# Optimization experiments

Measured on AMD Instinct MI355X. Metric: run time of the kernel, lower is better.

## Reference

```python
import jax, jax.numpy as jnp
import numpy as np

DIM = 128
IND_DIM = 5
HEADS = 4
DIM_HEAD = 32
HIDDEN = HEADS * DIM_HEAD  # 128
SCALE = DIM_HEAD ** -0.5


def setup_inputs() -> dict:
    key = jax.random.key(0)
    ks = jax.random.split(key, 6)
    b, n = 1, 512
    x = jax.random.normal(ks[0], (b, DIM, n), dtype=jnp.float32)
    indicator = jax.random.normal(ks[1], (b, IND_DIM, n, n), dtype=jnp.float32)
    # conv1d kernels with kernel_size=1 are just (out, in) matrices
    w_qkv = jax.random.normal(ks[2], (HIDDEN * 3, DIM), dtype=jnp.float32) * (DIM ** -0.5)
    w_ind = jax.random.normal(ks[3], (HIDDEN * 2, IND_DIM), dtype=jnp.float32) * (IND_DIM ** -0.5)
    w_out = jax.random.normal(ks[4], (DIM, HIDDEN), dtype=jnp.float32) * (HIDDEN ** -0.5)
    b_out = jax.random.normal(ks[5], (DIM,), dtype=jnp.float32) * 0.01
    return {"x": x, "indicator": indicator, "w_qkv": w_qkv,
            "w_ind": w_ind, "w_out": w_out, "b_out": b_out}


def reference(x, indicator, w_qkv, w_ind, w_out, b_out):
    b, c, n = x.shape
    h, dh = HEADS, DIM_HEAD
    # pointwise conv = channel matmul
    qkv = jnp.einsum('oc,bcn->bon', w_qkv, x)  # (b, 3*hidden, n)
    q, k, v = jnp.split(qkv, 3, axis=1)
    q = q.reshape(b, h, dh, n)
    k = k.reshape(b, h, dh, n)
    v = v.reshape(b, h, dh, n)
    ind = jnp.einsum('oc,bcij->boij', w_ind, indicator)  # (b, 2*hidden, n, n)
    ind_q, ind_k = jnp.split(ind, 2, axis=1)
    ind_q = ind_q.reshape(b, h, dh, n, n)
    ind_k = ind_k.reshape(b, h, dh, n, n)
    qq = (q[..., :, None] + ind_q) * SCALE        # (b, h, dh, n, n)
    kk = k[..., None, :] + ind_k                   # (b, h, dh, n, n)
    sim = jnp.einsum('bhdij,bhdij->bhij', qq, kk)  # (b, h, n, n)
    attn = jax.nn.softmax(sim, axis=-1)
    out = jnp.einsum('bhij,bhdj->bhdi', attn, v)   # (b, h, dh, n)
    out = out.reshape(b, h * dh, n)
    return jnp.einsum('oc,bcn->bon', w_out, out) + b_out[None, :, None]
```

## Files before the change

kernel.cpp:

```cpp
#include <hip/hip_runtime.h>
#include <hip/hip_fp16.h>
#include <math.h>

#define N      512
#define DIMC   128
#define HEADS  4
#define DH     32
#define INDC   5
#define SCALE  0.1767766952966369f

#define QKV_ROWS 384
#define AQ_BASE  384
#define AK_BASE  404
#define TOT_ROWS 424
#define NROW_BLK (TOT_ROWS / 4)

#define MHS_F    (TOT_ROWS * N / 2)
#define WOUTT_F  (MHS_F + 64)

__global__ __launch_bounds__(256) void pre_kernel(const float* __restrict__ w_qkv,
                                                  const float* __restrict__ w_ind,
                                                  const float* __restrict__ x,
                                                  const float* __restrict__ w_out,
                                                  float* __restrict__ ws) {
    const int bx = blockIdx.x;
    const int t  = threadIdx.x;
    __half* rows  = (__half*)ws;
    float* MhS    = ws + MHS_F;
    float* w_outT = ws + WOUTT_F;

    if (bx == NROW_BLK) {
        if (blockIdx.y != 0) return;
        __shared__ float mraw[HEADS * INDC * INDC];
        if (t < HEADS * INDC * INDC) {
            const int h = t / 25, c = (t / 5) % 5, cc = t % 5;
            float acc = 0.f;
            for (int d = 0; d < DH; ++d)
                acc = fmaf(w_ind[(h * DH + d) * INDC + c],
                           w_ind[(DIMC + h * DH + d) * INDC + cc], acc);
            mraw[t] = acc;
        }
        __syncthreads();
        if (t < 64) {
            const int h = t >> 4, idx = t & 15;
            const int PC[10]  = {0, 0, 0, 0, 1, 1, 1, 2, 2, 3};
            const int PCC[10] = {1, 2, 3, 4, 2, 3, 4, 3, 4, 4};
            float s = 0.f;
            if (idx < 5) {
                s = mraw[h * 25 + idx * 5 + idx];
            } else if (idx < 15) {
                const int c = PC[idx - 5], cc = PCC[idx - 5];
                s = mraw[h * 25 + c * 5 + cc] + mraw[h * 25 + cc * 5 + c];
            }
            MhS[h * 16 + idx] = s;
        }
        for (int idx = t; idx < DIMC * DIMC; idx += 256) {
            const int o = idx >> 7, c = idx & 127;
            w_outT[c * DIMC + o] = w_out[idx];
        }
        return;
    }

    __shared__ float ws2[4 * DIMC];
    const int o0 = bx * 4;
    for (int idx = t; idx < 4 * DIMC; idx += 256) {
        const int r = idx & 3, m = idx >> 2;
        const int row = o0 + r;
        float val;
        if (row < QKV_ROWS) {
            val = w_qkv[row * DIMC + m];
        } else if (row < AK_BASE) {
            const int rr = row - AQ_BASE, h = rr / INDC, c = rr % INDC;
            float acc = 0.f;
            for (int d = 0; d < DH; ++d)
                acc = fmaf(w_qkv[(h * DH + d) * DIMC + m],
                           w_ind[(DIMC + h * DH + d) * INDC + c], acc);
            val = acc;
        } else {
            const int rr = row - AK_BASE, h = rr / INDC, c = rr % INDC;
            float acc = 0.f;
            for (int d = 0; d < DH; ++d)
                acc = fmaf(w_qkv[(DIMC + h * DH + d) * DIMC + m],
                           w_ind[(h * DH + d) * INDC + c], acc);
            val = acc;
        }
        ws2[m * 4 + r] = val;
    }
    __syncthreads();

    const int i = blockIdx.y * 256 + t;
    float acc[4] = {0.f, 0.f, 0.f, 0.f};
#pragma unroll 8
    for (int c = 0; c < DIMC; ++c) {
        const float xv = x[c * N + i];
        const float4 wv = *(const float4*)(ws2 + c * 4);
        acc[0] = fmaf(wv.x, xv, acc[0]);
        acc[1] = fmaf(wv.y, xv, acc[1]);
        acc[2] = fmaf(wv.z, xv, acc[2]);
        acc[3] = fmaf(wv.w, xv, acc[3]);
    }
#pragma unroll
    for (int r = 0; r < 4; ++r) rows[(o0 + r) * N + i] = __float2half(acc[r]);
}

__global__ __launch_bounds__(256) void attn_kernel(const float* __restrict__ ws,
                                                   const float* __restrict__ ind,
                                                   const float* __restrict__ b_out,
                                                   float* __restrict__ out) {
    const int i0   = blockIdx.x * 2;
    const int t    = threadIdx.x;
    const int lane = t & 63;
    const int wave = t >> 6;

    const __half* rows  = (const __half*)ws;
    const float* MhS    = ws + MHS_F;
    const float* w_outT = ws + WOUTT_F;

    const __half* q  = rows;
    const __half* Aq = rows + 3 * DIMC * N;

    __shared__ float qs[2][DIMC];
    __shared__ float aqs[2][HEADS * INDC];
    __shared__ float msS[HEADS * 16];
    __shared__ float ps[HEADS][2][N];
    __shared__ float red[HEADS][DH][64];
    __shared__ float red4[2][HEADS][2][4];
    __shared__ float attv[2][DIMC];
    __shared__ float outred[4][2][DIMC];

    if (t < DIMC) qs[0][t] = __half2float(q[t * N + i0]);
    else          qs[1][t - DIMC] = __half2float(q[(t - DIMC) * N + i0 + 1]);
    if (t < 2 * HEADS * INDC) {
        const int ii = t / (HEADS * INDC), r = t % (HEADS * INDC);
        aqs[ii][r] = __half2float(Aq[r * N + i0 + ii]);
    } else if (t < 2 * HEADS * INDC + 64) {
        msS[t - 2 * HEADS * INDC] = MhS[t - 2 * HEADS * INDC];
    }
    __syncthreads();

    float2 ic0[INDC], ic1[INDC];
#pragma unroll
    for (int c = 0; c < INDC; ++c) {
        ic0[c] = ((const float2*)(ind + (c * N + i0) * N))[t];
        ic1[c] = ((const float2*)(ind + (c * N + i0 + 1) * N))[t];
    }
    float2 prod0[15], prod1[15];
#pragma unroll
    for (int c = 0; c < INDC; ++c) {
        prod0[c] = make_float2(ic0[c].x * ic0[c].x, ic0[c].y * ic0[c].y);
        prod1[c] = make_float2(ic1[c].x * ic1[c].x, ic1[c].y * ic1[c].y);
    }
    {
        int p = 5;
#pragma unroll
        for (int c = 0; c < INDC; ++c)
#pragma unroll
            for (int cc = c + 1; cc < INDC; ++cc, ++p) {
                prod0[p] = make_float2(ic0[c].x * ic0[cc].x, ic0[c].y * ic0[cc].y);
                prod1[p] = make_float2(ic1[c].x * ic1[cc].x, ic1[c].y * ic1[cc].y);
            }
    }

    const __half2* k2  = (const __half2*)(rows + DIMC * N);
    const __half2* Ak2 = (const __half2*)(rows + (3 * DIMC + HEADS * INDC) * N);
    float2 sim0[HEADS], sim1[HEADS];
#pragma unroll
    for (int h = 0; h < HEADS; ++h) {
        float2 qk0 = {0.f, 0.f}, qk1 = {0.f, 0.f};
#pragma unroll
        for (int d = 0; d < DH; ++d) {
            const float2 kv = __half22float2(k2[(h * DH + d) * 256 + t]);
            const float q0 = qs[0][h * DH + d], q1 = qs[1][h * DH + d];
            qk0.x = fmaf(q0, kv.x, qk0.x); qk0.y = fmaf(q0, kv.y, qk0.y);
            qk1.x = fmaf(q1, kv.x, qk1.x); qk1.y = fmaf(q1, kv.y, qk1.y);
        }
        float2 lin0 = {0.f, 0.f}, lin1 = {0.f, 0.f};
#pragma unroll
        for (int c = 0; c < INDC; ++c) {
            const float2 akv = __half22float2(Ak2[(h * INDC + c) * 256 + t]);
            const float a0 = aqs[0][h * INDC + c], a1 = aqs[1][h * INDC + c];
            lin0.x = fmaf(a0 + akv.x, ic0[c].x, lin0.x);
            lin0.y = fmaf(a0 + akv.y, ic0[c].y, lin0.y);
            lin1.x = fmaf(a1 + akv.x, ic1[c].x, lin1.x);
            lin1.y = fmaf(a1 + akv.y, ic1[c].y, lin1.y);
        }
        float2 qd0 = {0.f, 0.f}, qd1 = {0.f, 0.f};
#pragma unroll
        for (int p = 0; p < 15; ++p) {
            const float sv = msS[h * 16 + p];
            qd0.x = fmaf(sv, prod0[p].x, qd0.x); qd0.y = fmaf(sv, prod0[p].y, qd0.y);
            qd1.x = fmaf(sv, prod1[p].x, qd1.x); qd1.y = fmaf(sv, prod1[p].y, qd1.y);
        }
        sim0[h].x = SCALE * (qk0.x + lin0.x + qd0.x);
        sim0[h].y = SCALE * (qk0.y + lin0.y + qd0.y);
        sim1[h].x = SCALE * (qk1.x + lin1.x + qd1.x);
        sim1[h].y = SCALE * (qk1.y + lin1.y + qd1.y);
    }

#pragma unroll
    for (int h = 0; h < HEADS; ++h) {
        float m0 = fmaxf(sim0[h].x, sim0[h].y);
        float m1 = fmaxf(sim1[h].x, sim1[h].y);
#pragma unroll
        for (int off = 32; off; off >>= 1) {
            m0 = fmaxf(m0, __shfl_down(m0, off, 64));
            m1 = fmaxf(m1, __shfl_down(m1, off, 64));
        }
        if (lane == 0) { red4[0][h][0][wave] = m0; red4[0][h][1][wave] = m1; }
    }
    __syncthreads();
    float2 e0[HEADS], e1[HEADS];
#pragma unroll
    for (int h = 0; h < HEADS; ++h) {
        const float m0 = fmaxf(fmaxf(red4[0][h][0][0], red4[0][h][0][1]),
                               fmaxf(red4[0][h][0][2], red4[0][h][0][3]));
        const float m1 = fmaxf(fmaxf(red4[0][h][1][0], red4[0][h][1][1]),
                               fmaxf(red4[0][h][1][2], red4[0][h][1][3]));
        e0[h].x = __expf(sim0[h].x - m0); e0[h].y = __expf(sim0[h].y - m0);
        e1[h].x = __expf(sim1[h].x - m1); e1[h].y = __expf(sim1[h].y - m1);
        float s0 = e0[h].x + e0[h].y, s1 = e1[h].x + e1[h].y;
#pragma unroll
        for (int off = 32; off; off >>= 1) {
            s0 += __shfl_down(s0, off, 64);
            s1 += __shfl_down(s1, off, 64);
        }
        if (lane == 0) { red4[1][h][0][wave] = s0; red4[1][h][1][wave] = s1; }
    }
    __syncthreads();
#pragma unroll
    for (int h = 0; h < HEADS; ++h) {
        const float s0 = (red4[1][h][0][0] + red4[1][h][0][1]) +
                         (red4[1][h][0][2] + red4[1][h][0][3]);
        const float s1 = (red4[1][h][1][0] + red4[1][h][1][1]) +
                         (red4[1][h][1][2] + red4[1][h][1][3]);
        const float r0 = 1.f / s0, r1 = 1.f / s1;
        ((float2*)&ps[h][0][0])[t] = make_float2(e0[h].x * r0, e0[h].y * r0);
        ((float2*)&ps[h][1][0])[t] = make_float2(e1[h].x * r1, e1[h].y * r1);
    }
    __syncthreads();

    {
        const int h = wave;
        float acc0[DH], acc1[DH];
#pragma unroll
        for (int d = 0; d < DH; ++d) { acc0[d] = 0.f; acc1[d] = 0.f; }
        const float2* ps0 = (const float2*)&ps[h][0][0];
        const float2* ps1 = (const float2*)&ps[h][1][0];
        const __half2* v2 = (const __half2*)(rows + 2 * DIMC * N);
        for (int s = 0; s < 4; ++s) {
            const float2 p0 = ps0[lane + 64 * s];
            const float2 p1 = ps1[lane + 64 * s];
#pragma unroll
            for (int d = 0; d < DH; ++d) {
                const float2 vv = __half22float2(v2[(h * DH + d) * 256 + lane + 64 * s]);
                acc0[d] = fmaf(p0.x, vv.x, fmaf(p0.y, vv.y, acc0[d]));
                acc1[d] = fmaf(p1.x, vv.x, fmaf(p1.y, vv.y, acc1[d]));
            }
        }
        const int d = lane & 31, half = lane >> 5;
#pragma unroll
        for (int dd = 0; dd < DH; ++dd) red[h][dd][lane ^ dd] = acc0[dd];
        float s = 0.f;
#pragma unroll
        for (int kk = 0; kk < 32; ++kk) s += red[h][d][(half * 32 + kk) ^ d];
        s += __shfl_down(s, 32, 64);
        if (lane < 32) attv[0][h * DH + d] = s;
#pragma unroll
        for (int dd = 0; dd < DH; ++dd) red[h][dd][lane ^ dd] = acc1[dd];
        s = 0.f;
#pragma unroll
        for (int kk = 0; kk < 32; ++kk) s += red[h][d][(half * 32 + kk) ^ d];
        s += __shfl_down(s, 32, 64);
        if (lane < 32) attv[1][h * DH + d] = s;
    }
    __syncthreads();

    {
        const int po = t & 63;
        const int quarter = t >> 6;
        const float2* wT2 = (const float2*)w_outT;
        float2 a0 = {0.f, 0.f}, a1 = {0.f, 0.f};
#pragma unroll 8
        for (int c = quarter * 32; c < quarter * 32 + 32; ++c) {
            const float2 wv = wT2[c * 64 + po];
            const float av0 = attv[0][c], av1 = attv[1][c];
            a0.x = fmaf(wv.x, av0, a0.x); a0.y = fmaf(wv.y, av0, a0.y);
            a1.x = fmaf(wv.x, av1, a1.x); a1.y = fmaf(wv.y, av1, a1.y);
        }
        ((float2*)&outred[quarter][0][0])[po] = a0;
        ((float2*)&outred[quarter][1][0])[po] = a1;
    }
    __syncthreads();
    {
        const int o = t & 127, ii = t >> 7;
        out[o * N + i0 + ii] = ((outred[0][ii][o] + outred[1][ii][o]) +
                                (outred[2][ii][o] + outred[3][ii][o])) + b_out[o];
    }
}

extern "C" void kernel_launch(void* const* d_in, const int* in_sizes, int n_in,
                              void* d_out, int out_size, void* d_ws, size_t ws_size,
                              hipStream_t stream) {
    const float* x         = (const float*)d_in[0];
    const float* indicator = (const float*)d_in[1];
    const float* w_qkv     = (const float*)d_in[2];
    const float* w_ind     = (const float*)d_in[3];
    const float* w_out     = (const float*)d_in[4];
    const float* b_out     = (const float*)d_in[5];
    float* out = (float*)d_out;
    float* ws  = (float*)d_ws;

    pre_kernel<<<dim3(NROW_BLK + 1, 2), 256, 0, stream>>>(w_qkv, w_ind, x, w_out, ws);
    attn_kernel<<<N / 2, 256, 0, stream>>>(ws, indicator, b_out, out);
}
```

Baseline: 101.2 us.

## Assign one head per wave so softmax and PV stay in registers

Each wave now owns one head over all 512 keys, with four keys per lane loaded as float4 indicator values and packed half4 k/v. It computes the scores, the softmax with wave-level shuffles, and the PV accumulation directly from registers. This removes the shared-memory probability buffer, the cross-wave max/sum reductions and three block barriers. Normalisation is deferred to the final attention vector. In exchange, each wave recomputes the indicator products per head, and the larger per-lane register state may lower occupancy.

```diff
diff --git a/kernel.cpp b/kernel.cpp
--- a/kernel.cpp
+++ b/kernel.cpp
@@ -110,24 +110,32 @@
     const int i0   = blockIdx.x * 2;
     const int t    = threadIdx.x;
     const int lane = t & 63;
-    const int wave = t >> 6;
+    const int h    = t >> 6;
 
     const __half* rows  = (const __half*)ws;
     const float* MhS    = ws + MHS_F;
     const float* w_outT = ws + WOUTT_F;
 
-    const __half* q  = rows;
-    const __half* Aq = rows + 3 * DIMC * N;
-
     __shared__ float qs[2][DIMC];
     __shared__ float aqs[2][HEADS * INDC];
     __shared__ float msS[HEADS * 16];
-    __shared__ float ps[HEADS][2][N];
     __shared__ float red[HEADS][DH][64];
-    __shared__ float red4[2][HEADS][2][4];
     __shared__ float attv[2][DIMC];
     __shared__ float outred[4][2][DIMC];
 
+    float4 ic0[2][INDC], ic1[2][INDC];
+#pragma unroll
+    for (int s = 0; s < 2; ++s) {
+        const int g = lane + 64 * s;
+#pragma unroll
+        for (int c = 0; c < INDC; ++c) {
+            ic0[s][c] = ((const float4*)(ind + (c * N + i0) * N))[g];
+            ic1[s][c] = ((const float4*)(ind + (c * N + i0 + 1) * N))[g];
+        }
+    }
+
+    const __half* q  = rows;
+    const __half* Aq = rows + 3 * DIMC * N;
     if (t < DIMC) qs[0][t] = __half2float(q[t * N + i0]);
     else          qs[1][t - DIMC] = __half2float(q[(t - DIMC) * N + i0 + 1]);
     if (t < 2 * HEADS * INDC) {
@@ -138,125 +146,100 @@
     }
     __syncthreads();
 
-    float2 ic0[INDC], ic1[INDC];
-#pragma unroll
-    for (int c = 0; c < INDC; ++c) {
-        ic0[c] = ((const float2*)(ind + (c * N + i0) * N))[t];
-        ic1[c] = ((const float2*)(ind + (c * N + i0 + 1) * N))[t];
-    }
-    float2 prod0[15], prod1[15];
-#pragma unroll
-    for (int c = 0; c < INDC; ++c) {
-        prod0[c] = make_float2(ic0[c].x * ic0[c].x, ic0[c].y * ic0[c].y);
-        prod1[c] = make_float2(ic1[c].x * ic1[c].x, ic1[c].y * ic1[c].y);
-    }
-    {
-        int p = 5;
-#pragma unroll
-        for (int c = 0; c < INDC; ++c)
-#pragma unroll
-            for (int cc = c + 1; cc < INDC; ++cc, ++p) {
-                prod0[p] = make_float2(ic0[c].x * ic0[cc].x, ic0[c].y * ic0[cc].y);
-                prod1[p] = make_float2(ic1[c].x * ic1[cc].x, ic1[c].y * ic1[cc].y);
-            }
-    }
-
-    const __half2* k2  = (const __half2*)(rows + DIMC * N);
-    const __half2* Ak2 = (const __half2*)(rows + (3 * DIMC + HEADS * INDC) * N);
-    float2 sim0[HEADS], sim1[HEADS];
-#pragma unroll
-    for (int h = 0; h < HEADS; ++h) {
-        float2 qk0 = {0.f, 0.f}, qk1 = {0.f, 0.f};
+    const float2* k4  = (const float2*)(rows + DIMC * N);
+    const float2* v4  = (const float2*)(rows + 2 * DIMC * N);
+    const float2* Ak4 = (const float2*)(rows + (3 * DIMC + HEADS * INDC) * N);
+
+    float4 sr0[2], sr1[2];
+    float m0 = -1e30f, m1 = -1e30f;
+#pragma unroll
+    for (int s = 0; s < 2; ++s) {
+        const int g = lane + 64 * s;
+        float4 a0 = {0.f, 0.f, 0.f, 0.f}, a1 = {0.f, 0.f, 0.f, 0.f};
 #pragma unroll
         for (int d = 0; d < DH; ++d) {
-            const float2 kv = __half22float2(k2[(h * DH + d) * 256 + t]);
+            const float2 raw = k4[(h * DH + d) * 128 + g];
+            const float2 fa = __half22float2(*(const __half2*)&raw.x);
+            const float2 fb = __half22float2(*(const __half2*)&raw.y);
             const float q0 = qs[0][h * DH + d], q1 = qs[1][h * DH + d];
-            qk0.x = fmaf(q0, kv.x, qk0.x); qk0.y = fmaf(q0, kv.y, qk0.y);
-            qk1.x = fmaf(q1, kv.x, qk1.x); qk1.y = fmaf(q1, kv.y, qk1.y);
-        }
-        float2 lin0 = {0.f, 0.f}, lin1 = {0.f, 0.f};
+            a0.x = fmaf(q0, fa.x, a0.x); a0.y = fmaf(q0, fa.y, a0.y);
+            a0.z = fmaf(q0, fb.x, a0.z); a0.w = fmaf(q0, fb.y, a0.w);
+            a1.x = fmaf(q1, fa.x, a1.x); a1.y = fmaf(q1, fa.y, a1.y);
+            a1.z = fmaf(q1, fb.x, a1.z); a1.w = fmaf(q1, fb.y, a1.w);
+        }
 #pragma unroll
         for (int c = 0; c < INDC; ++c) {
-            const float2 akv = __half22float2(Ak2[(h * INDC + c) * 256 + t]);
-            const float a0 = aqs[0][h * INDC + c], a1 = aqs[1][h * INDC + c];
-            lin0.x = fmaf(a0 + akv.x, ic0[c].x, lin0.x);
-            lin0.y = fmaf(a0 + akv.y, ic0[c].y, lin0.y);
-            lin1.x = fmaf(a1 + akv.x, ic1[c].x, lin1.x);
-            lin1.y = fmaf(a1 + akv.y, ic1[c].y, lin1.y);
-        }
-        float2 qd0 = {0.f, 0.f}, qd1 = {0.f, 0.f};
+            const float2 raw = Ak4[(h * INDC + c) * 128 + g];
+            const float2 fa = __half22float2(*(const __half2*)&raw.x);
+            const float2 fb = __half22float2(*(const __half2*)&raw.y);
+            const float b0 = aqs[0][h * INDC + c], b1 = aqs[1][h * INDC + c];
+            const float4 v0 = ic0[s][c], v1 = ic1[s][c];
+            a0.x = fmaf(b0 + fa.x, v0.x, a0.x); a0.y = fmaf(b0 + fa.y, v0.y, a0.y);
+            a0.z = fmaf(b0 + fb.x, v0.z, a0.z); a0.w = fmaf(b0 + fb.y, v0.w, a0.w);
+            a1.x = fmaf(b1 + fa.x, v1.x, a1.x); a1.y = fmaf(b1 + fa.y, v1.y, a1.y);
+            a1.z = fmaf(b1 + fb.x, v1.z, a1.z); a1.w = fmaf(b1 + fb.y, v1.w, a1.w);
+        }
+        const int PCf[15]  = {0, 1, 2, 3, 4, 0, 0, 0, 0, 1, 1, 1, 2, 2, 3};
+        const int PCCf[15] = {0, 1, 2, 3, 4, 1, 2, 3, 4, 2, 3, 4, 3, 4, 4};
 #pragma unroll
         for (int p = 0; p < 15; ++p) {
             const float sv = msS[h * 16 + p];
-            qd0.x = fmaf(sv, prod0[p].x, qd0.x); qd0.y = fmaf(sv, prod0[p].y, qd0.y);
-            qd1.x = fmaf(sv, prod1[p].x, qd1.x); qd1.y = fmaf(sv, prod1[p].y, qd1.y);
-        }
-        sim0[h].x = SCALE * (qk0.x + lin0.x + qd0.x);
-        sim0[h].y = SCALE * (qk0.y + lin0.y + qd0.y);
-        sim1[h].x = SCALE * (qk1.x + lin1.x + qd1.x);
-        sim1[h].y = SCALE * (qk1.y + lin1.y + qd1.y);
-    }
-
-#pragma unroll
-    for (int h = 0; h < HEADS; ++h) {
-        float m0 = fmaxf(sim0[h].x, sim0[h].y);
-        float m1 = fmaxf(sim1[h].x, sim1[h].y);
-#pragma unroll
-        for (int off = 32; off; off >>= 1) {
-            m0 = fmaxf(m0, __shfl_down(m0, off, 64));
-            m1 = fmaxf(m1, __shfl_down(m1, off, 64));
-        }
-        if (lane == 0) { red4[0][h][0][wave] = m0; red4[0][h][1][wave] = m1; }
-    }
-    __syncthreads();
-    float2 e0[HEADS], e1[HEADS];
-#pragma unroll
-    for (int h = 0; h < HEADS; ++h) {
-        const float m0 = fmaxf(fmaxf(red4[0][h][0][0], red4[0][h][0][1]),
-                               fmaxf(red4[0][h][0][2], red4[0][h][0][3]));
-        const float m1 = fmaxf(fmaxf(red4[0][h][1][0], red4[0][h][1][1]),
-                               fmaxf(red4[0][h][1][2], red4[0][h][1][3]));
-        e0[h].x = __expf(sim0[h].x - m0); e0[h].y = __expf(sim0[h].y - m0);
-        e1[h].x = __expf(sim1[h].x - m1); e1[h].y = __expf(sim1[h].y - m1);
-        float s0 = e0[h].x + e0[h].y, s1 = e1[h].x + e1[h].y;
-#pragma unroll
-        for (int off = 32; off; off >>= 1) {
-            s0 += __shfl_down(s0, off, 64);
-            s1 += __shfl_down(s1, off, 64);
-        }
-        if (lane == 0) { red4[1][h][0][wave] = s0; red4[1][h][1][wave] = s1; }
-    }
-    __syncthreads();
-#pragma unroll
-    for (int h = 0; h < HEADS; ++h) {
-        const float s0 = (red4[1][h][0][0] + red4[1][h][0][1]) +
-                         (red4[1][h][0][2] + red4[1][h][0][3]);
-        const float s1 = (red4[1][h][1][0] + red4[1][h][1][1]) +
-                         (red4[1][h][1][2] + red4[1][h][1][3]);
-        const float r0 = 1.f / s0, r1 = 1.f / s1;
-        ((float2*)&ps[h][0][0])[t] = make_float2(e0[h].x * r0, e0[h].y * r0);
-        ((float2*)&ps[h][1][0])[t] = make_float2(e1[h].x * r1, e1[h].y * r1);
-    }
-    __syncthreads();
+            const float4 A0 = ic0[s][PCf[p]], B0 = ic0[s][PCCf[p]];
+            const float4 A1 = ic1[s][PCf[p]], B1 = ic1[s][PCCf[p]];
+            a0.x = fmaf(sv, A0.x * B0.x, a0.x); a0.y = fmaf(sv, A0.y * B0.y, a0.y);
+            a0.z = fmaf(sv, A0.z * B0.z, a0.z); a0.w = fmaf(sv, A0.w * B0.w, a0.w);
+            a1.x = fmaf(sv, A1.x * B1.x, a1.x); a1.y = fmaf(sv, A1.y * B1.y, a1.y);
+            a1.z = fmaf(sv, A1.z * B1.z, a1.z); a1.w = fmaf(sv, A1.w * B1.w, a1.w);
+        }
+        sr0[s] = make_float4(SCALE * a0.x, SCALE * a0.y, SCALE * a0.z, SCALE * a0.w);
+        sr1[s] = make_float4(SCALE * a1.x, SCALE * a1.y, SCALE * a1.z, SCALE * a1.w);
+        m0 = fmaxf(m0, fmaxf(fmaxf(sr0[s].x, sr0[s].y), fmaxf(sr0[s].z, sr0[s].w)));
+        m1 = fmaxf(m1, fmaxf(fmaxf(sr1[s].x, sr1[s].y), fmaxf(sr1[s].z, sr1[s].w)));
+    }
+
+#pragma unroll
+    for (int off = 1; off < 64; off <<= 1) {
+        m0 = fmaxf(m0, __shfl_xor(m0, off, 64));
+        m1 = fmaxf(m1, __shfl_xor(m1, off, 64));
+    }
+    float4 e0[2], e1[2];
+    float sum0 = 0.f, sum1 = 0.f;
+#pragma unroll
+    for (int s = 0; s < 2; ++s) {
+        e0[s].x = __expf(sr0[s].x - m0); e0[s].y = __expf(sr0[s].y - m0);
+        e0[s].z = __expf(sr0[s].z - m0); e0[s].w = __expf(sr0[s].w - m0);
+        e1[s].x = __expf(sr1[s].x - m1); e1[s].y = __expf(sr1[s].y - m1);
+        e1[s].z = __expf(sr1[s].z - m1); e1[s].w = __expf(sr1[s].w - m1);
+        sum0 += (e0[s].x + e0[s].y) + (e0[s].z + e0[s].w);
+        sum1 += (e1[s].x + e1[s].y) + (e1[s].z + e1[s].w);
+    }
+#pragma unroll
+    for (int off = 1; off < 64; off <<= 1) {
+        sum0 += __shfl_xor(sum0, off, 64);
+        sum1 += __shfl_xor(sum1, off, 64);
+    }
+    const float r0 = 1.f / sum0, r1 = 1.f / sum1;
+
+    float acc0[DH], acc1[DH];
+#pragma unroll
+    for (int d = 0; d < DH; ++d) { acc0[d] = 0.f; acc1[d] = 0.f; }
+#pragma unroll
+    for (int s = 0; s < 2; ++s) {
+        const int g = lane + 64 * s;
+        const float4 p0 = e0[s], p1 = e1[s];
+#pragma unroll
+        for (int d = 0; d < DH; ++d) {
+            const float2 raw = v4[(h * DH + d) * 128 + g];
+            const float2 fa = __half22float2(*(const __half2*)&raw.x);
+            const float2 fb = __half22float2(*(const __half2*)&raw.y);
+            acc0[d] = fmaf(p0.x, fa.x, fmaf(p0.y, fa.y,
+                      fmaf(p0.z, fb.x, fmaf(p0.w, fb.y, acc0[d]))));
+            acc1[d] = fmaf(p1.x, fa.x, fmaf(p1.y, fa.y,
+                      fmaf(p1.z, fb.x, fmaf(p1.w, fb.y, acc1[d]))));
+        }
+    }
 
     {
-        const int h = wave;
-        float acc0[DH], acc1[DH];
-#pragma unroll
-        for (int d = 0; d < DH; ++d) { acc0[d] = 0.f; acc1[d] = 0.f; }
-        const float2* ps0 = (const float2*)&ps[h][0][0];
-        const float2* ps1 = (const float2*)&ps[h][1][0];
-        const __half2* v2 = (const __half2*)(rows + 2 * DIMC * N);
-        for (int s = 0; s < 4; ++s) {
-            const float2 p0 = ps0[lane + 64 * s];
-            const float2 p1 = ps1[lane + 64 * s];
-#pragma unroll
-            for (int d = 0; d < DH; ++d) {
-                const float2 vv = __half22float2(v2[(h * DH + d) * 256 + lane + 64 * s]);
-                acc0[d] = fmaf(p0.x, vv.x, fmaf(p0.y, vv.y, acc0[d]));
-                acc1[d] = fmaf(p1.x, vv.x, fmaf(p1.y, vv.y, acc1[d]));
-            }
-        }
         const int d = lane & 31, half = lane >> 5;
 #pragma unroll
         for (int dd = 0; dd < DH; ++dd) red[h][dd][lane ^ dd] = acc0[dd];
@@ -264,14 +247,14 @@
 #pragma unroll
         for (int kk = 0; kk < 32; ++kk) s += red[h][d][(half * 32 + kk) ^ d];
         s += __shfl_down(s, 32, 64);
-        if (lane < 32) attv[0][h * DH + d] = s;
+        if (lane < 32) attv[0][h * DH + d] = s * r0;
 #pragma unroll
         for (int dd = 0; dd < DH; ++dd) red[h][dd][lane ^ dd] = acc1[dd];
         s = 0.f;
 #pragma unroll
         for (int kk = 0; kk < 32; ++kk) s += red[h][d][(half * 32 + kk) ^ d];
         s += __shfl_down(s, 32, 64);
-        if (lane < 32) attv[1][h * DH + d] = s;
+        if (lane < 32) attv[1][h * DH + d] = s * r1;
     }
     __syncthreads();
 
```

New measurement: 98.38 us. 1.03x faster.
